# Kernel optimization log

Measured on AMD Instinct MI355X. Metric: run time of the kernel, lower is better.

Reference implementation:

```python
import jax, jax.numpy as jnp
import numpy as np

B, N, DIM = 2, 8192, 3
K = 16            # num_neighbours (dilation=1)
R = 2048          # num_representitives
CIN, CL, COUT = 64, 16, 128
K2 = K * K


def _bn(x, g, b):
    # BatchNorm in eval mode with running_mean=0, running_var=1 -> affine
    return x * g + b


def setup_inputs() -> dict:
    key = jax.random.key(0)
    ks = jax.random.split(key, 24)
    r = lambda i, shape, s=1.0: jax.random.normal(ks[i], shape, jnp.float32) * s
    return {
        "points": r(0, (B, N, DIM)),
        "features": r(1, (B, N, CIN)),
        "lift_w": r(2, (CL, DIM), 0.3), "lift_b": r(3, (CL,), 0.1),
        "bn_lift_g": 1.0 + r(4, (CL,), 0.1), "bn_lift_b": r(5, (CL,), 0.1),
        "t1_w": r(6, (K2, DIM * K), 0.1), "t1_b": r(7, (K2,), 0.1),
        "bn1_g": 1.0 + r(8, (K2,), 0.1), "bn1_b": r(9, (K2,), 0.1),
        "t2_w": r(10, (K2, K2), 0.05), "t2_b": r(11, (K2,), 0.1),
        "bn2_g": 1.0 + r(12, (K2,), 0.1), "bn2_b": r(13, (K2,), 0.1),
        "t3_w": r(14, (K2, K2), 0.05), "t3_b": r(15, (K2,), 0.1),
        "bn3_g": 1.0 + r(16, (K2,), 0.1), "bn3_b": r(17, (K2,), 0.1),
        "conv_w": r(18, (COUT, CIN + CL, K), 0.05), "conv_b": r(19, (COUT,), 0.1),
        "rep_idx": jax.random.permutation(ks[20], N)[:R],
    }


def reference(points, features, lift_w, lift_b, bn_lift_g, bn_lift_b,
              t1_w, t1_b, bn1_g, bn1_b, t2_w, t2_b, bn2_g, bn2_b,
              t3_w, t3_b, bn3_g, bn3_b, conv_w, conv_b, rep_idx):
    b, n, _ = points.shape
    # ---- KNN (squared distance is order-equivalent to torch.cdist) ----
    sq = jnp.sum(points * points, -1)                                   # (b,n)
    d2 = sq[:, :, None] + sq[:, None, :] - 2.0 * jnp.einsum('bnd,bmd->bnm', points, points)
    _, idx = jax.lax.top_k(-d2, K + 1)                                  # (b,n,K+1)
    nn_idx = idx[:, :, 1:]                                              # drop self
    # ---- representative sampling + neighbor gather ----
    rep_pos = points[:, rep_idx]                                        # (b,R,3)
    nb_idx = nn_idx[:, rep_idx]                                         # (b,R,K)
    gather = jax.vmap(lambda arr, i: arr[i])
    nbr_pos = gather(points, nb_idx)                                    # (b,R,K,3)
    nbr_feat = gather(features, nb_idx)                                 # (b,R,K,CIN)
    # ---- X_conv ----
    p = (nbr_pos - rep_pos[:, :, None, :]).reshape(b * R, K, DIM)       # centered
    lifted = jax.nn.relu(_bn(p @ lift_w.T + lift_b, bn_lift_g, bn_lift_b))  # (bR,K,CL)
    feat = jnp.concatenate([lifted, nbr_feat.reshape(b * R, K, CIN)], -1)   # (bR,K,CL+CIN)
    pf = p.reshape(b * R, K * DIM)
    h = jax.nn.relu(_bn(pf @ t1_w.T + t1_b, bn1_g, bn1_b))
    h = jax.nn.relu(_bn(h @ t2_w.T + t2_b, bn2_g, bn2_b))
    T = _bn(h @ t3_w.T + t3_b, bn3_g, bn3_b).reshape(b * R, K, K)       # learned transform
    Tf = jnp.einsum('bij,bjc->bic', T, feat)                            # bmm, (bR,K,C)
    # Conv1d(C, COUT, kernel=K) over length K -> single output position
    out = jnp.einsum('bkc,ock->bo', Tf, conv_w) + conv_b                # (bR,COUT)
    return rep_pos, out.reshape(b, R, COUT)
```

## Files before the change

kernel.cpp:

```cpp
#include <hip/hip_runtime.h>
#include <float.h>

#define Bn 2
#define Nn 8192
#define Rr 2048
#define Kk 16
#define CIN 64
#define CL 16
#define COUT 128
#define K2c 256
#define GT (Bn*Rr)
#define FD (CL+CIN)
#define KC (Kk*FD)
#define MG 4

__global__ __launch_bounds__(256) void prep_kernel(
    const float* __restrict__ t1_w, const float* __restrict__ t2_w,
    const float* __restrict__ t3_w, const float* __restrict__ conv_w,
    const float* __restrict__ points,
    float* __restrict__ t1t, float* __restrict__ t2t,
    float* __restrict__ t3t, float* __restrict__ wp,
    float4* __restrict__ pts4)
{
  int i = blockIdx.x * 256 + threadIdx.x;
  if (i < K2c*48) { int j = i / 48, k = i - j*48; t1t[k*K2c + j] = t1_w[i]; }
  if (i < K2c*K2c) { int j = i >> 8, k = i & 255; t2t[k*K2c + j] = t2_w[i]; t3t[k*K2c + j] = t3_w[i]; }
  if (i < COUT*KC) {
    int o = i / KC, ck = i - o*KC;
    int c = ck >> 4, k = ck & 15;
    wp[(k*FD + c)*COUT + o] = conv_w[i];
  }
  if (i < Bn*Nn) {
    float x = points[i*3+0], y = points[i*3+1], z = points[i*3+2];
    float sq = __fadd_rn(__fadd_rn(__fmul_rn(x,x), __fmul_rn(y,y)), __fmul_rn(z,z));
    pts4[i] = make_float4(x, y, z, sq);
  }
}

__global__ __launch_bounds__(512) void knn_kernel(
    const float4* __restrict__ pts4, const int* __restrict__ rep_idx,
    int* __restrict__ nb_idx, float* __restrict__ p_out,
    float* __restrict__ rep_pos_out)
{
  __shared__ float4 ptsS[2048];
  __shared__ unsigned long long coll[8][128];
  int t    = threadIdx.x;
  int lane = t & 63;
  int w    = t >> 6;
  int g    = blockIdx.x * 8 + w;
  int b    = g >> 11;
  int r    = g & 2047;
  int n    = rep_idx[r];
  const float4* pb4 = pts4 + (size_t)b*Nn;
  float4 Q = pb4[n];
  float qx = Q.x, qy = Q.y, qz = Q.z, sqn = Q.w;

  float c0 = FLT_MAX, c1 = FLT_MAX, c2 = FLT_MAX;
  for (int c = 0; c < 4; c++) {
    int base = c * 2048;
    __syncthreads();
    for (int i = t; i < 2048; i += 512) ptsS[i] = pb4[base + i];
    __syncthreads();
    #pragma unroll 4
    for (int j = 0; j < 32; j++) {
      float4 P = ptsS[j*64 + lane];
      float dot = __fmaf_rn(qz, P.z, __fmaf_rn(qy, P.y, __fmul_rn(qx, P.x)));
      float d2  = __fsub_rn(__fadd_rn(sqn, P.w), __fmul_rn(2.0f, dot));
      float nc2 = __builtin_amdgcn_fmed3f(c1, c2, d2);
      float nc1 = __builtin_amdgcn_fmed3f(c0, c1, d2);
      float nc0 = fminf(c0, d2);
      c0 = nc0; c1 = nc1; c2 = nc2;
    }
  }

  float tau = FLT_MAX;
  for (int rnd = 0; rnd < 6; rnd++) {
    float m = c2;
    #pragma unroll
    for (int off = 1; off < 64; off <<= 1) m = fminf(m, __shfl_xor(m, off));
    if (c2 == m) c2 = FLT_MAX;
    tau = m;
  }

  int cnt = 0;
  #pragma unroll
  for (int cc = 0; cc < 4; cc++) {
    int c = (cc == 0) ? 3 : (cc - 1);
    int base = c * 2048;
    if (cc != 0) {
      __syncthreads();
      for (int i = t; i < 2048; i += 512) ptsS[i] = pb4[base + i];
      __syncthreads();
    }
    #pragma unroll 4
    for (int j = 0; j < 32; j++) {
      float4 P = ptsS[j*64 + lane];
      float dot = __fmaf_rn(qz, P.z, __fmaf_rn(qy, P.y, __fmul_rn(qx, P.x)));
      float d2  = __fsub_rn(__fadd_rn(sqn, P.w), __fmul_rn(2.0f, dot));
      bool pr = (d2 <= tau);
      unsigned long long mask = __ballot(pr);
      if (pr) {
        int pos = cnt + (int)__popcll(mask & ((1ull << lane) - 1ull));
        if (pos < 128) {
          unsigned f = __float_as_uint(d2);
          unsigned mono = f ^ ((unsigned)((int)f >> 31) | 0x80000000u);
          coll[w][pos] = ((unsigned long long)mono << 32) | (unsigned)(base + j*64 + lane);
        }
      }
      cnt += (int)__popcll(mask);
    }
  }
  if (cnt > 128) cnt = 128;

  unsigned long long e1 = (lane < cnt)      ? coll[w][lane]      : ~0ull;
  unsigned long long e2 = (lane + 64 < cnt) ? coll[w][lane + 64] : ~0ull;
  int out_m = 0;
  for (int rnd = 0; rnd < 17; rnd++) {
    unsigned long long myk = (e1 < e2) ? e1 : e2;
    unsigned long long kmin = myk;
    #pragma unroll
    for (int off = 1; off < 64; off <<= 1) {
      unsigned long long o = __shfl_xor(kmin, off);
      kmin = (o < kmin) ? o : kmin;
    }
    if (rnd >= 1 && lane == rnd - 1) out_m = (int)(kmin & 0xFFFFFFFFull);
    if (kmin == e1) e1 = ~0ull;
    else if (kmin == e2) e2 = ~0ull;
  }

  if (lane < 16) {
    nb_idx[g*Kk + lane] = out_m;
    float4 P = pb4[out_m];
    p_out[(g*Kk + lane)*3 + 0] = __fsub_rn(P.x, qx);
    p_out[(g*Kk + lane)*3 + 1] = __fsub_rn(P.y, qy);
    p_out[(g*Kk + lane)*3 + 2] = __fsub_rn(P.z, qz);
  }
  if (lane < 3) rep_pos_out[g*3 + lane] = (lane == 0 ? qx : (lane == 1 ? qy : qz));
}

__device__ __forceinline__ void fma_g(float4& a, float hv, const float4& wv) {
  a.x = fmaf(hv, wv.x, a.x);
  a.y = fmaf(hv, wv.y, a.y);
  a.z = fmaf(hv, wv.z, a.z);
  a.w = fmaf(hv, wv.w, a.w);
}

__global__ __launch_bounds__(256) void mlp_kernel(
    const float* __restrict__ p,
    const float* __restrict__ t1t, const float* __restrict__ t1_b,
    const float* __restrict__ g1v, const float* __restrict__ b1v,
    const float* __restrict__ t2t, const float* __restrict__ t2_b,
    const float* __restrict__ g2v, const float* __restrict__ b2v,
    const float* __restrict__ t3t, const float* __restrict__ t3_b,
    const float* __restrict__ g3v, const float* __restrict__ b3v,
    float* __restrict__ T_out)
{
  __shared__ float pf[48][MG];
  __shared__ float hA[K2c][MG];
  __shared__ float red[4*16*66];
  int t = threadIdx.x;
  int w = t >> 6, l = t & 63;
  int g0 = blockIdx.x * MG;
  for (int e = t; e < MG*48; e += 256) {
    int g = e / 48, k = e - g*48;
    pf[k][g] = p[(size_t)(g0+g)*48 + k];
  }
  __syncthreads();

  float4 acc[MG];

#define LDW(WSRC, K) (*(const float4*)&WSRC[(size_t)(K)*K2c + 4*l])

#define KSTAGE(WSRC, KDIM, HBUF, WB, KK, KNEXT)                        \
  {                                                                    \
    float4 wc = WB;                                                    \
    if ((KNEXT) < KDIM) WB = LDW(WSRC, KNEXT);                         \
    float4 h = *(const float4*)&HBUF[KK][0];                           \
    fma_g(acc[0], h.x, wc); fma_g(acc[1], h.y, wc);                    \
    fma_g(acc[2], h.z, wc); fma_g(acc[3], h.w, wc);                    \
  }

#define KLOOP(WSRC, KDIM, HBUF)                                        \
  {                                                                    \
    _Pragma("unroll")                                                  \
    for (int q = 0; q < MG; q++) acc[q] = make_float4(0.f,0.f,0.f,0.f);\
    float4 wb0 = LDW(WSRC, w);                                         \
    float4 wb1 = (w + 4  < KDIM) ? LDW(WSRC, w + 4)  : wb0;            \
    float4 wb2 = (w + 8  < KDIM) ? LDW(WSRC, w + 8)  : wb0;            \
    float4 wb3 = (w + 12 < KDIM) ? LDW(WSRC, w + 12) : wb0;            \
    for (int k = w; k < KDIM; k += 16) {                               \
      KSTAGE(WSRC, KDIM, HBUF, wb0, k,      k + 16)                    \
      if (k + 4 < KDIM)  KSTAGE(WSRC, KDIM, HBUF, wb1, k + 4,  k + 20) \
      if (k + 8 < KDIM)  KSTAGE(WSRC, KDIM, HBUF, wb2, k + 8,  k + 24) \
      if (k + 12 < KDIM) KSTAGE(WSRC, KDIM, HBUF, wb3, k + 12, k + 28) \
    }                                                                  \
  }

#define WRITE_RED()                                                    \
  {                                                                    \
    _Pragma("unroll")                                                  \
    for (int q = 0; q < MG; q++) {                                     \
      red[(w*16 + 0*4 + q)*66 + l] = acc[q].x;                         \
      red[(w*16 + 1*4 + q)*66 + l] = acc[q].y;                         \
      red[(w*16 + 2*4 + q)*66 + l] = acc[q].z;                         \
      red[(w*16 + 3*4 + q)*66 + l] = acc[q].w;                         \
    }                                                                  \
  }

#define REDUCE(S)                                                      \
  float4 S = make_float4(0.f,0.f,0.f,0.f);                             \
  {                                                                    \
    int lr = t >> 2, cc = t & 3;                                       \
    _Pragma("unroll")                                                  \
    for (int ww = 0; ww < 4; ww++) {                                   \
      S.x += red[(ww*16 + cc*4 + 0)*66 + lr];                          \
      S.y += red[(ww*16 + cc*4 + 1)*66 + lr];                          \
      S.z += red[(ww*16 + cc*4 + 2)*66 + lr];                          \
      S.w += red[(ww*16 + cc*4 + 3)*66 + lr];                          \
    }                                                                  \
  }

  KLOOP(t1t, 48, pf)
  WRITE_RED()
  __syncthreads();
  {
    REDUCE(s)
    float bb = t1_b[t], gg = g1v[t], oo = b1v[t];
    float4 v;
    v.x = fmaxf(fmaf(s.x + bb, gg, oo), 0.f);
    v.y = fmaxf(fmaf(s.y + bb, gg, oo), 0.f);
    v.z = fmaxf(fmaf(s.z + bb, gg, oo), 0.f);
    v.w = fmaxf(fmaf(s.w + bb, gg, oo), 0.f);
    *(float4*)&hA[t][0] = v;
  }
  __syncthreads();

  KLOOP(t2t, K2c, hA)
  WRITE_RED()
  __syncthreads();
  {
    REDUCE(s)
    float bb = t2_b[t], gg = g2v[t], oo = b2v[t];
    float4 v;
    v.x = fmaxf(fmaf(s.x + bb, gg, oo), 0.f);
    v.y = fmaxf(fmaf(s.y + bb, gg, oo), 0.f);
    v.z = fmaxf(fmaf(s.z + bb, gg, oo), 0.f);
    v.w = fmaxf(fmaf(s.w + bb, gg, oo), 0.f);
    *(float4*)&hA[t][0] = v;
  }
  __syncthreads();

  KLOOP(t3t, K2c, hA)
  WRITE_RED()
  __syncthreads();
  {
    REDUCE(s)
    float bb = t3_b[t], gg = g3v[t], oo = b3v[t];
    T_out[(size_t)(g0+0)*K2c + t] = fmaf(s.x + bb, gg, oo);
    T_out[(size_t)(g0+1)*K2c + t] = fmaf(s.y + bb, gg, oo);
    T_out[(size_t)(g0+2)*K2c + t] = fmaf(s.z + bb, gg, oo);
    T_out[(size_t)(g0+3)*K2c + t] = fmaf(s.w + bb, gg, oo);
  }
#undef KLOOP
#undef KSTAGE
#undef LDW
#undef WRITE_RED
#undef REDUCE
}

__global__ __launch_bounds__(256) void tf_kernel(
    const float* __restrict__ T_in, const float* __restrict__ features,
    const float* __restrict__ p, const int* __restrict__ nb_idx,
    const float* __restrict__ lift_w, const float* __restrict__ lift_b,
    const float* __restrict__ bng, const float* __restrict__ bnb,
    float* __restrict__ Tf)
{
  __shared__ float T_s[4*K2c];
  __shared__ float f_s[4*KC];
  __shared__ float ps[4*48];
  __shared__ int   idxs[64];
  __shared__ float lw[48], lb2[16], lg[16], lo[16];
  int t = threadIdx.x;
  int g0 = blockIdx.x * 4;
  int b = g0 / Rr;
  for (int e = t; e < 4*K2c; e += 256) T_s[e] = T_in[(size_t)g0*K2c + e];
  if (t >= 32 && t < 224) {
    int e = t - 32;
    ps[e] = p[(size_t)g0*48 + e];
  }
  if (t < 64) idxs[t] = nb_idx[g0*16 + t];
  if (t >= 64 && t < 112)  lw[t-64]   = lift_w[t-64];
  if (t >= 112 && t < 128) lb2[t-112] = lift_b[t-112];
  if (t >= 224 && t < 240) lg[t-224]  = bng[t-224];
  if (t >= 240)            lo[t-240]  = bnb[t-240];
  __syncthreads();

  {
    int wv = t >> 6, ln = t & 63;
    for (int row = wv; row < 64; row += 4) {
      int gg = row >> 4, k = row & 15;
      f_s[gg*KC + k*FD + CL + ln] = features[((size_t)b*Nn + idxs[row])*CIN + ln];
    }
  }
  for (int e = t; e < 1024; e += 256) {
    int gg = e >> 8, rem = e & 255, k = rem >> 4, c = rem & 15;
    float acc = ps[gg*48 + k*3 + 0]*lw[c*3+0] + ps[gg*48 + k*3 + 1]*lw[c*3+1]
              + ps[gg*48 + k*3 + 2]*lw[c*3+2] + lb2[c];
    acc = acc*lg[c] + lo[c];
    f_s[gg*KC + k*FD + c] = fmaxf(acc, 0.f);
  }
  __syncthreads();

  int gg = t >> 6;
  int cl = t & 63;
  for (int ci = cl; ci < FD; ci += 64) {
    float fcol[16];
    #pragma unroll
    for (int j = 0; j < 16; j++) fcol[j] = f_s[gg*KC + j*FD + ci];
    #pragma unroll
    for (int k = 0; k < 16; k++) {
      float acc = 0.f;
      #pragma unroll
      for (int j = 0; j < 16; j++) acc = fmaf(T_s[gg*K2c + k*16 + j], fcol[j], acc);
      Tf[(size_t)(g0+gg)*KC + k*FD + ci] = acc;
    }
  }
}

__global__ __launch_bounds__(256) void gemm_kernel(
    const float* __restrict__ A,
    const float* __restrict__ Bm,
    float* __restrict__ part)
{
  __shared__ float As[16*36];
  __shared__ float Bs[16*COUT];
  int t = threadIdx.x;
  int m0 = blockIdx.x * 32;
  int ky = blockIdx.y;
  int kbase0 = ky * (KC/8);
  float acc[4][4];
  #pragma unroll
  for (int i = 0; i < 4; i++)
    #pragma unroll
    for (int j = 0; j < 4; j++) acc[i][j] = 0.f;
  int tn = t & 31, tm = t >> 5;

  for (int kt = 0; kt < KC/8; kt += 16) {
    int kb = kbase0 + kt;
    {
      int kcol = t & 15, row = t >> 4;
      As[kcol*36 + row]      = A[(size_t)(m0+row)*KC + kb + kcol];
      As[kcol*36 + row + 16] = A[(size_t)(m0+row+16)*KC + kb + kcol];
    }
    {
      int o = t & 127, kk2 = t >> 7;
      #pragma unroll
      for (int p4 = 0; p4 < 8; p4++) {
        int kk = kk2 + p4*2;
        Bs[kk*COUT + o] = Bm[(size_t)(kb+kk)*COUT + o];
      }
    }
    __syncthreads();
    #pragma unroll
    for (int kk = 0; kk < 16; kk++) {
      float4 a4 = *(const float4*)&As[kk*36 + tm*4];
      float4 b4 = *(const float4*)&Bs[kk*COUT + tn*4];
      float av[4] = {a4.x, a4.y, a4.z, a4.w};
      float bv[4] = {b4.x, b4.y, b4.z, b4.w};
      #pragma unroll
      for (int i = 0; i < 4; i++)
        #pragma unroll
        for (int j = 0; j < 4; j++) acc[i][j] = fmaf(av[i], bv[j], acc[i][j]);
    }
    __syncthreads();
  }
  #pragma unroll
  for (int i = 0; i < 4; i++) {
    float4 v = make_float4(acc[i][0], acc[i][1], acc[i][2], acc[i][3]);
    *(float4*)&part[((size_t)ky*GT + m0 + tm*4 + i)*COUT + tn*4] = v;
  }
}

__global__ __launch_bounds__(256) void reduce_kernel(
    const float* __restrict__ part, const float* __restrict__ conv_b,
    float* __restrict__ outp)
{
  int i = blockIdx.x*256 + threadIdx.x;
  float4 s = ((const float4*)conv_b)[i & 31];
  #pragma unroll
  for (int w = 0; w < 8; w++) {
    float4 v = ((const float4*)(part + (size_t)w*GT*COUT))[i];
    s.x += v.x; s.y += v.y; s.z += v.z; s.w += v.w;
  }
  ((float4*)outp)[i] = s;
}

extern "C" void kernel_launch(void* const* d_in, const int* in_sizes, int n_in,
                              void* d_out, int out_size, void* d_ws, size_t ws_size,
                              hipStream_t stream) {
  const float* points   = (const float*)d_in[0];
  const float* features = (const float*)d_in[1];
  const float* lift_w   = (const float*)d_in[2];
  const float* lift_b   = (const float*)d_in[3];
  const float* bn_lift_g= (const float*)d_in[4];
  const float* bn_lift_b= (const float*)d_in[5];
  const float* t1_w     = (const float*)d_in[6];
  const float* t1_b     = (const float*)d_in[7];
  const float* bn1_g    = (const float*)d_in[8];
  const float* bn1_b    = (const float*)d_in[9];
  const float* t2_w     = (const float*)d_in[10];
  const float* t2_b     = (const float*)d_in[11];
  const float* bn2_g    = (const float*)d_in[12];
  const float* bn2_b    = (const float*)d_in[13];
  const float* t3_w     = (const float*)d_in[14];
  const float* t3_b     = (const float*)d_in[15];
  const float* bn3_g    = (const float*)d_in[16];
  const float* bn3_b    = (const float*)d_in[17];
  const float* conv_w   = (const float*)d_in[18];
  const float* conv_b   = (const float*)d_in[19];
  const int*   rep_idx  = (const int*)d_in[20];

  char* ws = (char*)d_ws;
  int*    nb   = (int*)   (ws + 0);
  float*  p    = (float*) (ws + 262144);
  float*  T    = (float*) (ws + 1048576);
  float*  Tf   = (float*) (ws + 5242880);
  float*  wp   = (float*) (ws + 26214400);
  float*  t1t  = (float*) (ws + 26869760);
  float*  t2t  = (float*) (ws + 26918912);
  float*  t3t  = (float*) (ws + 27181056);
  float*  part = (float*) (ws + 33554432);
  float4* pts4 = (float4*)(ws + 52428800);

  float* rep_pos = (float*)d_out;
  float* outp    = (float*)d_out + (size_t)GT*3;

  prep_kernel<<<640, 256, 0, stream>>>(t1_w, t2_w, t3_w, conv_w, points,
                                       t1t, t2t, t3t, wp, pts4);
  knn_kernel<<<GT/8, 512, 0, stream>>>(pts4, rep_idx, nb, p, rep_pos);
  mlp_kernel<<<GT/MG, 256, 0, stream>>>(p, t1t, t1_b, bn1_g, bn1_b,
                                        t2t, t2_b, bn2_g, bn2_b,
                                        t3t, t3_b, bn3_g, bn3_b, T);
  tf_kernel<<<GT/4, 256, 0, stream>>>(T, features, p, nb,
                                      lift_w, lift_b, bn_lift_g, bn_lift_b, Tf);
  dim3 ggrid(GT/32, 8);
  gemm_kernel<<<ggrid, 256, 0, stream>>>(Tf, wp, part);
  reduce_kernel<<<(GT*COUT/4)/256, 256, 0, stream>>>(part, conv_b, outp);
}
```

Before: 218.1 us.

## Share each staged point across eight queries per thread in KNN kernel

Restructures the KNN kernel so every thread keeps eight queries in registers and checks each shared-memory point against all eight queries at once, rather than one wave handling one query. This cuts LDS reads per distance eightfold. Per-thread top-3 candidates are merged through shared memory to get a per-query threshold. Candidate collection now uses shared-memory atomics into a 192-slot buffer instead of ballot compaction. The costs are higher register pressure, extra merge and sync steps, and atomic contention during collection.

```diff
diff --git a/kernel.cpp b/kernel.cpp
--- a/kernel.cpp
+++ b/kernel.cpp
@@ -13,6 +13,7 @@
 #define FD (CL+CIN)
 #define KC (Kk*FD)
 #define MG 4
+#define CCAP 192
 
 __global__ __launch_bounds__(256) void prep_kernel(
     const float* __restrict__ t1_w, const float* __restrict__ t2_w,
@@ -37,86 +38,149 @@
   }
 }
 
-__global__ __launch_bounds__(512) void knn_kernel(
+__global__ __launch_bounds__(512, 4) void knn_kernel(
     const float4* __restrict__ pts4, const int* __restrict__ rep_idx,
     int* __restrict__ nb_idx, float* __restrict__ p_out,
     float* __restrict__ rep_pos_out)
 {
-  __shared__ float4 ptsS[2048];
-  __shared__ unsigned long long coll[8][128];
+  union SmemU {
+    float4 ptsS[2048];
+    float  cbuf[8][1536];
+  };
+  __shared__ SmemU U;
+  __shared__ unsigned long long coll[8][CCAP];
+  __shared__ float4 qS[8];
+  __shared__ float  tauS[8];
+  __shared__ int    ccnt[8];
+
   int t    = threadIdx.x;
   int lane = t & 63;
   int w    = t >> 6;
-  int g    = blockIdx.x * 8 + w;
-  int b    = g >> 11;
-  int r    = g & 2047;
-  int n    = rep_idx[r];
+  int g0   = blockIdx.x * 8;
+  int b    = g0 >> 11;
   const float4* pb4 = pts4 + (size_t)b*Nn;
-  float4 Q = pb4[n];
-  float qx = Q.x, qy = Q.y, qz = Q.z, sqn = Q.w;
-
-  float c0 = FLT_MAX, c1 = FLT_MAX, c2 = FLT_MAX;
+
+  if (t < 8) {
+    int g = g0 + t;
+    int r = g & 2047;
+    qS[t] = pb4[rep_idx[r]];
+    ccnt[t] = 0;
+  }
+  __syncthreads();
+
+  float qx[8], qy[8], qz[8], qw[8];
+  #pragma unroll
+  for (int q = 0; q < 8; q++) {
+    float4 Q = qS[q];
+    qx[q] = __uint_as_float(__builtin_amdgcn_readfirstlane(__float_as_uint(Q.x)));
+    qy[q] = __uint_as_float(__builtin_amdgcn_readfirstlane(__float_as_uint(Q.y)));
+    qz[q] = __uint_as_float(__builtin_amdgcn_readfirstlane(__float_as_uint(Q.z)));
+    qw[q] = __uint_as_float(__builtin_amdgcn_readfirstlane(__float_as_uint(Q.w)));
+  }
+
+  float c0[8], c1[8], c2[8];
+  #pragma unroll
+  for (int q = 0; q < 8; q++) { c0[q] = FLT_MAX; c1[q] = FLT_MAX; c2[q] = FLT_MAX; }
+
   for (int c = 0; c < 4; c++) {
     int base = c * 2048;
     __syncthreads();
-    for (int i = t; i < 2048; i += 512) ptsS[i] = pb4[base + i];
+    for (int i = t; i < 2048; i += 512) U.ptsS[i] = pb4[base + i];
     __syncthreads();
-    #pragma unroll 4
-    for (int j = 0; j < 32; j++) {
-      float4 P = ptsS[j*64 + lane];
-      float dot = __fmaf_rn(qz, P.z, __fmaf_rn(qy, P.y, __fmul_rn(qx, P.x)));
-      float d2  = __fsub_rn(__fadd_rn(sqn, P.w), __fmul_rn(2.0f, dot));
-      float nc2 = __builtin_amdgcn_fmed3f(c1, c2, d2);
-      float nc1 = __builtin_amdgcn_fmed3f(c0, c1, d2);
-      float nc0 = fminf(c0, d2);
-      c0 = nc0; c1 = nc1; c2 = nc2;
-    }
-  }
-
-  float tau = FLT_MAX;
-  for (int rnd = 0; rnd < 6; rnd++) {
-    float m = c2;
-    #pragma unroll
-    for (int off = 1; off < 64; off <<= 1) m = fminf(m, __shfl_xor(m, off));
-    if (c2 == m) c2 = FLT_MAX;
-    tau = m;
-  }
-
-  int cnt = 0;
-  #pragma unroll
-  for (int cc = 0; cc < 4; cc++) {
-    int c = (cc == 0) ? 3 : (cc - 1);
+    #pragma unroll
+    for (int j = 0; j < 4; j++) {
+      float4 P = U.ptsS[j*512 + t];
+      #pragma unroll
+      for (int q = 0; q < 8; q++) {
+        float dot = __fmaf_rn(qz[q], P.z, __fmaf_rn(qy[q], P.y, __fmul_rn(qx[q], P.x)));
+        float d2  = __fsub_rn(__fadd_rn(qw[q], P.w), __fmul_rn(2.0f, dot));
+        float nc2 = __builtin_amdgcn_fmed3f(c1[q], c2[q], d2);
+        float nc1 = __builtin_amdgcn_fmed3f(c0[q], c1[q], d2);
+        float nc0 = fminf(c0[q], d2);
+        c0[q] = nc0; c1[q] = nc1; c2[q] = nc2;
+      }
+    }
+  }
+
+  __syncthreads();
+  #pragma unroll
+  for (int q = 0; q < 8; q++) {
+    U.cbuf[q][0*512 + t] = c0[q];
+    U.cbuf[q][1*512 + t] = c1[q];
+    U.cbuf[q][2*512 + t] = c2[q];
+  }
+  __syncthreads();
+
+  {
+    float C0 = FLT_MAX, C1 = FLT_MAX, C2 = FLT_MAX;
+    #pragma unroll
+    for (int j = 0; j < 8; j++) {
+      int s = lane + 64*j;
+      #pragma unroll
+      for (int i = 0; i < 3; i++) {
+        float v = U.cbuf[w][i*512 + s];
+        float n2 = __builtin_amdgcn_fmed3f(C1, C2, v);
+        float n1 = __builtin_amdgcn_fmed3f(C0, C1, v);
+        float n0 = fminf(C0, v);
+        C0 = n0; C1 = n1; C2 = n2;
+      }
+    }
+    float tw = FLT_MAX;
+    #pragma unroll
+    for (int rnd = 0; rnd < 6; rnd++) {
+      float m = C2;
+      #pragma unroll
+      for (int off = 1; off < 64; off <<= 1) m = fminf(m, __shfl_xor(m, off));
+      if (C2 == m) C2 = FLT_MAX;
+      tw = m;
+    }
+    if (lane == 0) tauS[w] = tw;
+  }
+  __syncthreads();
+
+  float tau[8];
+  #pragma unroll
+  for (int q = 0; q < 8; q++)
+    tau[q] = __uint_as_float(__builtin_amdgcn_readfirstlane(__float_as_uint(tauS[q])));
+
+  for (int c = 0; c < 4; c++) {
     int base = c * 2048;
-    if (cc != 0) {
-      __syncthreads();
-      for (int i = t; i < 2048; i += 512) ptsS[i] = pb4[base + i];
-      __syncthreads();
-    }
-    #pragma unroll 4
-    for (int j = 0; j < 32; j++) {
-      float4 P = ptsS[j*64 + lane];
-      float dot = __fmaf_rn(qz, P.z, __fmaf_rn(qy, P.y, __fmul_rn(qx, P.x)));
-      float d2  = __fsub_rn(__fadd_rn(sqn, P.w), __fmul_rn(2.0f, dot));
-      bool pr = (d2 <= tau);
-      unsigned long long mask = __ballot(pr);
-      if (pr) {
-        int pos = cnt + (int)__popcll(mask & ((1ull << lane) - 1ull));
-        if (pos < 128) {
-          unsigned f = __float_as_uint(d2);
-          unsigned mono = f ^ ((unsigned)((int)f >> 31) | 0x80000000u);
-          coll[w][pos] = ((unsigned long long)mono << 32) | (unsigned)(base + j*64 + lane);
+    __syncthreads();
+    for (int i = t; i < 2048; i += 512) U.ptsS[i] = pb4[base + i];
+    __syncthreads();
+    #pragma unroll
+    for (int j = 0; j < 4; j++) {
+      float4 P = U.ptsS[j*512 + t];
+      int idx = base + j*512 + t;
+      #pragma unroll
+      for (int q = 0; q < 8; q++) {
+        float dot = __fmaf_rn(qz[q], P.z, __fmaf_rn(qy[q], P.y, __fmul_rn(qx[q], P.x)));
+        float d2  = __fsub_rn(__fadd_rn(qw[q], P.w), __fmul_rn(2.0f, dot));
+        if (d2 <= tau[q]) {
+          int pos = atomicAdd(&ccnt[q], 1);
+          if (pos < CCAP) {
+            unsigned f = __float_as_uint(d2);
+            unsigned mono = f ^ ((unsigned)((int)f >> 31) | 0x80000000u);
+            coll[q][pos] = ((unsigned long long)mono << 32) | (unsigned)idx;
+          }
         }
       }
-      cnt += (int)__popcll(mask);
-    }
-  }
-  if (cnt > 128) cnt = 128;
-
-  unsigned long long e1 = (lane < cnt)      ? coll[w][lane]      : ~0ull;
-  unsigned long long e2 = (lane + 64 < cnt) ? coll[w][lane + 64] : ~0ull;
+    }
+  }
+  __syncthreads();
+
+  int cnt = ccnt[w];
+  if (cnt > CCAP) cnt = CCAP;
+  const unsigned long long* cw = coll[w];
+  unsigned long long e[3];
+  #pragma unroll
+  for (int k = 0; k < 3; k++)
+    e[k] = (lane + 64*k < cnt) ? cw[lane + 64*k] : ~0ull;
+
   int out_m = 0;
   for (int rnd = 0; rnd < 17; rnd++) {
-    unsigned long long myk = (e1 < e2) ? e1 : e2;
+    unsigned long long a01 = (e[0] < e[1]) ? e[0] : e[1];
+    unsigned long long myk = (a01 < e[2]) ? a01 : e[2];
     unsigned long long kmin = myk;
     #pragma unroll
     for (int off = 1; off < 64; off <<= 1) {
@@ -124,18 +188,21 @@
       kmin = (o < kmin) ? o : kmin;
     }
     if (rnd >= 1 && lane == rnd - 1) out_m = (int)(kmin & 0xFFFFFFFFull);
-    if (kmin == e1) e1 = ~0ull;
-    else if (kmin == e2) e2 = ~0ull;
-  }
-
+    if      (kmin == e[0]) e[0] = ~0ull;
+    else if (kmin == e[1]) e[1] = ~0ull;
+    else if (kmin == e[2]) e[2] = ~0ull;
+  }
+
+  int g = g0 + w;
+  float4 Q = qS[w];
   if (lane < 16) {
     nb_idx[g*Kk + lane] = out_m;
     float4 P = pb4[out_m];
-    p_out[(g*Kk + lane)*3 + 0] = __fsub_rn(P.x, qx);
-    p_out[(g*Kk + lane)*3 + 1] = __fsub_rn(P.y, qy);
-    p_out[(g*Kk + lane)*3 + 2] = __fsub_rn(P.z, qz);
-  }
-  if (lane < 3) rep_pos_out[g*3 + lane] = (lane == 0 ? qx : (lane == 1 ? qy : qz));
+    p_out[(g*Kk + lane)*3 + 0] = __fsub_rn(P.x, Q.x);
+    p_out[(g*Kk + lane)*3 + 1] = __fsub_rn(P.y, Q.y);
+    p_out[(g*Kk + lane)*3 + 2] = __fsub_rn(P.z, Q.z);
+  }
+  if (lane < 3) rep_pos_out[g*3 + lane] = (lane == 0 ? Q.x : (lane == 1 ? Q.y : Q.z));
 }
 
 __device__ __forceinline__ void fma_g(float4& a, float hv, const float4& wv) {
```

Measured after the change: 217.3 us. Within noise of the previous version (-0.3%).
